# Performance work log

Hardware: AMD Instinct MI355X
Metric: run time of the kernel (lower is better)

The kernel has to match this reference:

```python
import jax, jax.numpy as jnp
import numpy as np

TOPOLOGY = [-1, 0, 0, 0, 1, 2, 3, 4, 5, 6, 7, 8, 9, 9, 9, 12, 13, 14, 16, 17, 18, 19, 20, 21]
JOINT_WEIGHTS = np.ones(24, dtype=np.float32)
B1 = 1.0
B2 = 1.0


def quaternion_to_matrix(q):
    # pytorch3d convention: real part first (w, x, y, z)
    w, x, y, z = q[..., 0], q[..., 1], q[..., 2], q[..., 3]
    two_s = 2.0 / jnp.sum(q * q, axis=-1)
    o = jnp.stack([
        1 - two_s * (y * y + z * z), two_s * (x * y - z * w), two_s * (x * z + y * w),
        two_s * (x * y + z * w), 1 - two_s * (x * x + z * z), two_s * (y * z - x * w),
        two_s * (x * z - y * w), two_s * (y * z + x * w), 1 - two_s * (x * x + y * y),
    ], axis=-1)
    return o.reshape(q.shape[:-1] + (3, 3))


def fk(topology, X_m, X_t):
    # X_m: (bs, T, J*4+3), X_t: (bs, J, 3)
    J = len(topology)
    quat = X_m[..., :-3].reshape(X_m.shape[:-1] + (J, 4))
    local_rot = quaternion_to_matrix(quat)          # (bs, T, J, 3, 3)
    grots = [None] * J
    gtrs = [None] * J
    grots[0] = local_rot[..., 0, :, :]
    gtrs[0] = X_m[..., -3:]                          # root translation
    for i in range(1, J):
        pi = topology[i]
        grots[i] = jnp.matmul(grots[pi], local_rot[..., i, :, :])
        gtrs[i] = jnp.einsum('btij,bj->bti', grots[pi], X_t[:, i]) + gtrs[pi]
    return jnp.stack(grots, axis=-3), jnp.stack(gtrs, axis=-2)


def split_raw_motion(raw_motion):
    position = raw_motion[..., -3:]
    rotation = raw_motion[..., :-3]
    rotation = rotation.reshape(rotation.shape[:-1] + (-1, 4))
    norm = jnp.linalg.norm(rotation, axis=-1, keepdims=True)
    rotation = rotation / jnp.maximum(norm, 1e-12)
    return rotation, position


def weighted_mse(w, a, b):
    # w: (J,), a/b: (bs, T, J, C) -> per-joint weighted mean squared error
    return jnp.mean(w[None, None, :, None] * (a - b) ** 2)


def setup_inputs() -> dict:
    key = jax.random.key(0)
    k1, k2, k3, k4 = jax.random.split(key, 4)
    bs, T, J = 64, 2048, 24
    return {
        'Y_m': jax.random.normal(k1, (bs, T, J * 4 + 3), dtype=jnp.float32),
        'X_m': jax.random.normal(k2, (bs, T, J * 4 + 3), dtype=jnp.float32),
        'Y_t': jax.random.normal(k3, (bs, J, 3), dtype=jnp.float32),
        'X_t': jax.random.normal(k4, (bs, J, 3), dtype=jnp.float32),
    }


def reference(Y_m, X_m, Y_t, X_t):
    w = jnp.asarray(JOINT_WEIGHTS)
    rot_x, pos_x = split_raw_motion(X_m)
    rot_y, pos_y = split_raw_motion(Y_m)
    grot_y, gtr_y = fk(TOPOLOGY, Y_m, Y_t)
    grot_x, gtr_x = fk(TOPOLOGY, X_m, X_t)
    loss_rot = B1 * weighted_mse(w, rot_y, rot_x)
    loss_fk = B2 * (2.5 * weighted_mse(w, gtr_y, gtr_x)
                    + jnp.mean((pos_y - pos_x) ** 2))
    return loss_rot + loss_fk
```

## Files before the change

kernel.cpp:

```cpp
#include <hip/hip_runtime.h>

#define BS 64
#define TT 2048
#define NJ 24
#define ROWF 99
#define BLOCK 128
#define NROWS (BS * TT)

__device__ __forceinline__ void ld4u(const float* __restrict__ p, float* q) {
  const float4 v = *reinterpret_cast<const float4*>(p);
  q[0] = v.x; q[1] = v.y; q[2] = v.z; q[3] = v.w;
}

__device__ __forceinline__ void quat2mat_s(const float* q, float s, float* R) {
  const float w = q[0], x = q[1], y = q[2], z = q[3];
  const float xx = s*x*x, yy = s*y*y, zz = s*z*z;
  const float xy = s*x*y, xz = s*x*z, yz = s*y*z;
  const float xw = s*x*w, yw = s*y*w, zw = s*z*w;
  R[0] = 1.0f - (yy+zz); R[1] = xy - zw;        R[2] = xz + yw;
  R[3] = xy + zw;        R[4] = 1.0f - (xx+zz); R[5] = yz - xw;
  R[6] = xz - yw;        R[7] = yz + xw;        R[8] = 1.0f - (xx+yy);
}

__device__ __forceinline__ void mm3(const float* A, const float* B, float* C) {
#pragma unroll
  for (int r = 0; r < 3; ++r) {
#pragma unroll
    for (int c = 0; c < 3; ++c) {
      C[3*r+c] = fmaf(A[3*r], B[c], fmaf(A[3*r+1], B[3+c], A[3*r+2]*B[6+c]));
    }
  }
}

__global__ __launch_bounds__(BLOCK, 2) void motion_loss_kernel(
    const float* __restrict__ Ym, const float* __restrict__ Xm,
    const float* __restrict__ Yt, const float* __restrict__ Xt,
    float* __restrict__ out) {
  const int tid = threadIdx.x;
  const size_t row = (size_t)blockIdx.x * BLOCK + tid;
  const int b = (int)(row / TT);
  const float* __restrict__ xr = Xm + row * ROWF;
  const float* __restrict__ yr = Ym + row * ROWF;
  const float* __restrict__ tX = Xt + (size_t)b * NJ * 3;
  const float* __restrict__ tY = Yt + (size_t)b * NJ * 3;

  float GX[3][9], GY[3][9], D[3][3];
  float rot_acc = 0.0f, gtr_acc = 0.0f, pos_acc = 0.0f;

  {
    float xq[4], yq[4];
    ld4u(xr, xq); ld4u(yr, yq);
    const float qqx = xq[0]*xq[0] + xq[1]*xq[1] + xq[2]*xq[2] + xq[3]*xq[3];
    const float qqy = yq[0]*yq[0] + yq[1]*yq[1] + yq[2]*yq[2] + yq[3]*yq[3];
    const float ix = 1.0f / fmaxf(sqrtf(qqx), 1e-12f);
    const float iy = 1.0f / fmaxf(sqrtf(qqy), 1e-12f);
    const float r0 = yq[0]*iy - xq[0]*ix, r1 = yq[1]*iy - xq[1]*ix;
    const float r2 = yq[2]*iy - xq[2]*ix, r3 = yq[3]*iy - xq[3]*ix;
    rot_acc += r0*r0 + r1*r1 + r2*r2 + r3*r3;
    quat2mat_s(xq, 2.0f / qqx, GX[0]);
    quat2mat_s(yq, 2.0f / qqy, GY[0]);
    float xp[4], yp[4];
    ld4u(xr + 95, xp); ld4u(yr + 95, yp);
    D[0][0] = yp[1] - xp[1]; D[0][1] = yp[2] - xp[2]; D[0][2] = yp[3] - xp[3];
    const float d2 = D[0][0]*D[0][0] + D[0][1]*D[0][1] + D[0][2]*D[0][2];
    gtr_acc += d2;
    pos_acc = d2;
  }

#define JSTEP(j, PS, NS) do {                                                  \
    float xq[4], yq[4];                                                        \
    ld4u(xr + 4*(j), xq); ld4u(yr + 4*(j), yq);                                \
    const float qqx = xq[0]*xq[0] + xq[1]*xq[1] + xq[2]*xq[2] + xq[3]*xq[3];   \
    const float qqy = yq[0]*yq[0] + yq[1]*yq[1] + yq[2]*yq[2] + yq[3]*yq[3];   \
    const float ix = 1.0f / fmaxf(sqrtf(qqx), 1e-12f);                         \
    const float iy = 1.0f / fmaxf(sqrtf(qqy), 1e-12f);                         \
    const float r0 = yq[0]*iy - xq[0]*ix, r1 = yq[1]*iy - xq[1]*ix;            \
    const float r2 = yq[2]*iy - xq[2]*ix, r3 = yq[3]*iy - xq[3]*ix;            \
    rot_acc += r0*r0 + r1*r1 + r2*r2 + r3*r3;                                  \
    const float tx0 = tX[3*(j)], tx1 = tX[3*(j)+1], tx2 = tX[3*(j)+2];         \
    const float ty0 = tY[3*(j)], ty1 = tY[3*(j)+1], ty2 = tY[3*(j)+2];         \
    const float vx0 = fmaf(GX[PS][0],tx0, fmaf(GX[PS][1],tx1, GX[PS][2]*tx2)); \
    const float vx1 = fmaf(GX[PS][3],tx0, fmaf(GX[PS][4],tx1, GX[PS][5]*tx2)); \
    const float vx2 = fmaf(GX[PS][6],tx0, fmaf(GX[PS][7],tx1, GX[PS][8]*tx2)); \
    const float vy0 = fmaf(GY[PS][0],ty0, fmaf(GY[PS][1],ty1, GY[PS][2]*ty2)); \
    const float vy1 = fmaf(GY[PS][3],ty0, fmaf(GY[PS][4],ty1, GY[PS][5]*ty2)); \
    const float vy2 = fmaf(GY[PS][6],ty0, fmaf(GY[PS][7],ty1, GY[PS][8]*ty2)); \
    const float d0 = D[PS][0] + (vy0 - vx0);                                   \
    const float d1 = D[PS][1] + (vy1 - vx1);                                   \
    const float d2 = D[PS][2] + (vy2 - vx2);                                   \
    gtr_acc += d0*d0 + d1*d1 + d2*d2;                                          \
    float RX[9], RY[9], GnX[9], GnY[9];                                        \
    quat2mat_s(xq, 2.0f / qqx, RX);                                            \
    quat2mat_s(yq, 2.0f / qqy, RY);                                            \
    mm3(GX[PS], RX, GnX);                                                      \
    mm3(GY[PS], RY, GnY);                                                      \
    _Pragma("unroll")                                                          \
    for (int k = 0; k < 9; ++k) { GX[NS][k] = GnX[k]; GY[NS][k] = GnY[k]; }    \
    D[NS][0] = d0; D[NS][1] = d1; D[NS][2] = d2;                               \
  } while (0)

  JSTEP( 1, 0, 1);
  JSTEP( 2, 0, 2);
  JSTEP( 3, 0, 0);
  JSTEP( 4, 1, 1);
  JSTEP( 5, 2, 2);
  JSTEP( 6, 0, 0);
  JSTEP( 7, 1, 1);
  JSTEP( 8, 2, 2);
  JSTEP( 9, 0, 0);
  JSTEP(10, 1, 1);
  JSTEP(11, 2, 2);
  JSTEP(12, 0, 1);
  JSTEP(13, 0, 2);
  JSTEP(14, 0, 0);
  JSTEP(15, 1, 1);
  JSTEP(16, 2, 2);
  JSTEP(17, 0, 0);
  JSTEP(18, 2, 2);
  JSTEP(19, 0, 0);
  JSTEP(20, 2, 2);
  JSTEP(21, 0, 0);
  JSTEP(22, 2, 2);
  JSTEP(23, 0, 0);
#undef JSTEP

  const float c_rot = 1.0f / ((float)NROWS * NJ * 4);
  const float c_gtr = 2.5f / ((float)NROWS * NJ * 3);
  const float c_pos = 1.0f / ((float)NROWS * 3);
  float contrib = c_rot * rot_acc + c_gtr * gtr_acc + c_pos * pos_acc;
#pragma unroll
  for (int o = 32; o > 0; o >>= 1) contrib += __shfl_down(contrib, o, 64);
  if ((tid & 63) == 0) atomicAdd(out, contrib);
}

extern "C" void kernel_launch(void* const* d_in, const int* in_sizes, int n_in,
                              void* d_out, int out_size, void* d_ws, size_t ws_size,
                              hipStream_t stream) {
  const float* Ym = (const float*)d_in[0];
  const float* Xm = (const float*)d_in[1];
  const float* Yt = (const float*)d_in[2];
  const float* Xt = (const float*)d_in[3];
  float* out = (float*)d_out;
  hipMemsetAsync(out, 0, sizeof(float), stream);
  motion_loss_kernel<<<NROWS / BLOCK, BLOCK, 0, stream>>>(Ym, Xm, Yt, Xt, out);
}
```

Baseline: 169.5 us.

## Split X and Y forward kinematics across paired lanes with shuffle differences

Each row is now handled by two adjacent lanes, one walking the X skeleton and one the Y skeleton. The lanes exchange normalized quaternions and joint positions with xor-shuffles to form the differences, and the loss weights are halved because each pair counts its result twice. Per-thread register state drops by about half and twice as many threads run, which should raise occupancy and memory-level parallelism. Bone offsets are staged in shared memory. The cost is extra shuffles per joint, duplicated difference arithmetic, and a strided per-lane access pattern over two input arrays.

```diff
diff --git a/kernel.cpp b/kernel.cpp
--- a/kernel.cpp
+++ b/kernel.cpp
@@ -4,7 +4,8 @@
 #define TT 2048
 #define NJ 24
 #define ROWF 99
-#define BLOCK 128
+#define BLOCK 256
+#define RPB (BLOCK / 2)
 #define NROWS (BS * TT)
 
 __device__ __forceinline__ void ld4u(const float* __restrict__ p, float* q) {
@@ -32,71 +33,72 @@
   }
 }
 
-__global__ __launch_bounds__(BLOCK, 2) void motion_loss_kernel(
+__global__ __launch_bounds__(BLOCK, 4) void motion_loss_kernel(
     const float* __restrict__ Ym, const float* __restrict__ Xm,
     const float* __restrict__ Yt, const float* __restrict__ Xt,
     float* __restrict__ out) {
+  __shared__ float ts[2][NJ * 3];
+
   const int tid = threadIdx.x;
-  const size_t row = (size_t)blockIdx.x * BLOCK + tid;
-  const int b = (int)(row / TT);
-  const float* __restrict__ xr = Xm + row * ROWF;
-  const float* __restrict__ yr = Ym + row * ROWF;
-  const float* __restrict__ tX = Xt + (size_t)b * NJ * 3;
-  const float* __restrict__ tY = Yt + (size_t)b * NJ * 3;
+  const int side = tid & 1;
+  const size_t row = (size_t)blockIdx.x * RPB + (tid >> 1);
+  const int b = (int)(((size_t)blockIdx.x * RPB) / TT);
 
-  float GX[3][9], GY[3][9], D[3][3];
+  if (tid < NJ * 3)                        ts[0][tid]       = Xt[(size_t)b * NJ * 3 + tid];
+  else if (tid >= 128 && tid < 128 + NJ*3) ts[1][tid - 128] = Yt[(size_t)b * NJ * 3 + (tid - 128)];
+  __syncthreads();
+
+  const float* __restrict__ mr = (side ? Ym : Xm) + row * ROWF;
+  const float* __restrict__ tv = ts[side];
+
+  float G[3][9], gtr[3][3];
   float rot_acc = 0.0f, gtr_acc = 0.0f, pos_acc = 0.0f;
 
   {
-    float xq[4], yq[4];
-    ld4u(xr, xq); ld4u(yr, yq);
-    const float qqx = xq[0]*xq[0] + xq[1]*xq[1] + xq[2]*xq[2] + xq[3]*xq[3];
-    const float qqy = yq[0]*yq[0] + yq[1]*yq[1] + yq[2]*yq[2] + yq[3]*yq[3];
-    const float ix = 1.0f / fmaxf(sqrtf(qqx), 1e-12f);
-    const float iy = 1.0f / fmaxf(sqrtf(qqy), 1e-12f);
-    const float r0 = yq[0]*iy - xq[0]*ix, r1 = yq[1]*iy - xq[1]*ix;
-    const float r2 = yq[2]*iy - xq[2]*ix, r3 = yq[3]*iy - xq[3]*ix;
+    float q[4]; ld4u(mr, q);
+    const float qq = q[0]*q[0] + q[1]*q[1] + q[2]*q[2] + q[3]*q[3];
+    const float in = 1.0f / fmaxf(sqrtf(qq), 1e-12f);
+    const float n0 = q[0]*in, n1 = q[1]*in, n2 = q[2]*in, n3 = q[3]*in;
+    const float r0 = n0 - __shfl_xor(n0, 1, 64);
+    const float r1 = n1 - __shfl_xor(n1, 1, 64);
+    const float r2 = n2 - __shfl_xor(n2, 1, 64);
+    const float r3 = n3 - __shfl_xor(n3, 1, 64);
     rot_acc += r0*r0 + r1*r1 + r2*r2 + r3*r3;
-    quat2mat_s(xq, 2.0f / qqx, GX[0]);
-    quat2mat_s(yq, 2.0f / qqy, GY[0]);
-    float xp[4], yp[4];
-    ld4u(xr + 95, xp); ld4u(yr + 95, yp);
-    D[0][0] = yp[1] - xp[1]; D[0][1] = yp[2] - xp[2]; D[0][2] = yp[3] - xp[3];
-    const float d2 = D[0][0]*D[0][0] + D[0][1]*D[0][1] + D[0][2]*D[0][2];
-    gtr_acc += d2;
-    pos_acc = d2;
+    quat2mat_s(q, 2.0f / qq, G[0]);
+    float p[4]; ld4u(mr + 95, p);
+    gtr[0][0] = p[1]; gtr[0][1] = p[2]; gtr[0][2] = p[3];
+    const float d0 = gtr[0][0] - __shfl_xor(gtr[0][0], 1, 64);
+    const float d1 = gtr[0][1] - __shfl_xor(gtr[0][1], 1, 64);
+    const float d2 = gtr[0][2] - __shfl_xor(gtr[0][2], 1, 64);
+    const float dd = d0*d0 + d1*d1 + d2*d2;
+    gtr_acc += dd;
+    pos_acc  = dd;
   }
 
 #define JSTEP(j, PS, NS) do {                                                  \
-    float xq[4], yq[4];                                                        \
-    ld4u(xr + 4*(j), xq); ld4u(yr + 4*(j), yq);                                \
-    const float qqx = xq[0]*xq[0] + xq[1]*xq[1] + xq[2]*xq[2] + xq[3]*xq[3];   \
-    const float qqy = yq[0]*yq[0] + yq[1]*yq[1] + yq[2]*yq[2] + yq[3]*yq[3];   \
-    const float ix = 1.0f / fmaxf(sqrtf(qqx), 1e-12f);                         \
-    const float iy = 1.0f / fmaxf(sqrtf(qqy), 1e-12f);                         \
-    const float r0 = yq[0]*iy - xq[0]*ix, r1 = yq[1]*iy - xq[1]*ix;            \
-    const float r2 = yq[2]*iy - xq[2]*ix, r3 = yq[3]*iy - xq[3]*ix;            \
+    float q[4]; ld4u(mr + 4*(j), q);                                           \
+    const float qq = q[0]*q[0] + q[1]*q[1] + q[2]*q[2] + q[3]*q[3];            \
+    const float in = 1.0f / fmaxf(sqrtf(qq), 1e-12f);                          \
+    const float n0 = q[0]*in, n1 = q[1]*in, n2 = q[2]*in, n3 = q[3]*in;        \
+    const float r0 = n0 - __shfl_xor(n0, 1, 64);                               \
+    const float r1 = n1 - __shfl_xor(n1, 1, 64);                               \
+    const float r2 = n2 - __shfl_xor(n2, 1, 64);                               \
+    const float r3 = n3 - __shfl_xor(n3, 1, 64);                               \
     rot_acc += r0*r0 + r1*r1 + r2*r2 + r3*r3;                                  \
-    const float tx0 = tX[3*(j)], tx1 = tX[3*(j)+1], tx2 = tX[3*(j)+2];         \
-    const float ty0 = tY[3*(j)], ty1 = tY[3*(j)+1], ty2 = tY[3*(j)+2];         \
-    const float vx0 = fmaf(GX[PS][0],tx0, fmaf(GX[PS][1],tx1, GX[PS][2]*tx2)); \
-    const float vx1 = fmaf(GX[PS][3],tx0, fmaf(GX[PS][4],tx1, GX[PS][5]*tx2)); \
-    const float vx2 = fmaf(GX[PS][6],tx0, fmaf(GX[PS][7],tx1, GX[PS][8]*tx2)); \
-    const float vy0 = fmaf(GY[PS][0],ty0, fmaf(GY[PS][1],ty1, GY[PS][2]*ty2)); \
-    const float vy1 = fmaf(GY[PS][3],ty0, fmaf(GY[PS][4],ty1, GY[PS][5]*ty2)); \
-    const float vy2 = fmaf(GY[PS][6],ty0, fmaf(GY[PS][7],ty1, GY[PS][8]*ty2)); \
-    const float d0 = D[PS][0] + (vy0 - vx0);                                   \
-    const float d1 = D[PS][1] + (vy1 - vx1);                                   \
-    const float d2 = D[PS][2] + (vy2 - vx2);                                   \
+    const float t0 = tv[3*(j)], t1 = tv[3*(j)+1], t2 = tv[3*(j)+2];            \
+    const float v0 = fmaf(G[PS][0],t0, fmaf(G[PS][1],t1, fmaf(G[PS][2],t2, gtr[PS][0]))); \
+    const float v1 = fmaf(G[PS][3],t0, fmaf(G[PS][4],t1, fmaf(G[PS][5],t2, gtr[PS][1]))); \
+    const float v2 = fmaf(G[PS][6],t0, fmaf(G[PS][7],t1, fmaf(G[PS][8],t2, gtr[PS][2]))); \
+    const float d0 = v0 - __shfl_xor(v0, 1, 64);                               \
+    const float d1 = v1 - __shfl_xor(v1, 1, 64);                               \
+    const float d2 = v2 - __shfl_xor(v2, 1, 64);                               \
     gtr_acc += d0*d0 + d1*d1 + d2*d2;                                          \
-    float RX[9], RY[9], GnX[9], GnY[9];                                        \
-    quat2mat_s(xq, 2.0f / qqx, RX);                                            \
-    quat2mat_s(yq, 2.0f / qqy, RY);                                            \
-    mm3(GX[PS], RX, GnX);                                                      \
-    mm3(GY[PS], RY, GnY);                                                      \
+    float R[9], Gn[9];                                                         \
+    quat2mat_s(q, 2.0f / qq, R);                                               \
+    mm3(G[PS], R, Gn);                                                         \
     _Pragma("unroll")                                                          \
-    for (int k = 0; k < 9; ++k) { GX[NS][k] = GnX[k]; GY[NS][k] = GnY[k]; }    \
-    D[NS][0] = d0; D[NS][1] = d1; D[NS][2] = d2;                               \
+    for (int k = 0; k < 9; ++k) G[NS][k] = Gn[k];                              \
+    gtr[NS][0] = v0; gtr[NS][1] = v1; gtr[NS][2] = v2;                         \
   } while (0)
 
   JSTEP( 1, 0, 1);
@@ -124,9 +126,9 @@
   JSTEP(23, 0, 0);
 #undef JSTEP
 
-  const float c_rot = 1.0f / ((float)NROWS * NJ * 4);
-  const float c_gtr = 2.5f / ((float)NROWS * NJ * 3);
-  const float c_pos = 1.0f / ((float)NROWS * 3);
+  const float c_rot = 0.5f / ((float)NROWS * NJ * 4);
+  const float c_gtr = 1.25f / ((float)NROWS * NJ * 3);
+  const float c_pos = 0.5f / ((float)NROWS * 3);
   float contrib = c_rot * rot_acc + c_gtr * gtr_acc + c_pos * pos_acc;
 #pragma unroll
   for (int o = 32; o > 0; o >>= 1) contrib += __shfl_down(contrib, o, 64);
@@ -142,5 +144,5 @@
   const float* Xt = (const float*)d_in[3];
   float* out = (float*)d_out;
   hipMemsetAsync(out, 0, sizeof(float), stream);
-  motion_loss_kernel<<<NROWS / BLOCK, BLOCK, 0, stream>>>(Ym, Xm, Yt, Xt, out);
+  motion_loss_kernel<<<NROWS / RPB, BLOCK, 0, stream>>>(Ym, Xm, Yt, Xt, out);
 }
```

Result: slower. 198.4 us (+17.0%).

## Split each row's kinematic tree across two wavefronts and stage offsets in LDS

Applied to the files above, without the earlier changes.

Each motion row is now handled by two threads in different wavefronts. One walks the spine and the left and right arm chains, the other walks the two leg chains after recomputing the shared spine prefix (joints 3, 6, 9) without accumulating. This shortens the serial dependency chain per thread, cuts live rotation state from three to two matrices, and allows four blocks per SM in the launch bounds. The per-batch joint offsets are staged in shared memory. The cost is the redundant spine recomputation and duplicate loads of the root quaternion and position.

```diff
diff --git a/kernel.cpp b/kernel.cpp
--- a/kernel.cpp
+++ b/kernel.cpp
@@ -4,7 +4,8 @@
 #define TT 2048
 #define NJ 24
 #define ROWF 99
-#define BLOCK 128
+#define BLOCK 256
+#define RPB 128
 #define NROWS (BS * TT)
 
 __device__ __forceinline__ void ld4u(const float* __restrict__ p, float* q) {
@@ -32,51 +33,50 @@
   }
 }
 
-__global__ __launch_bounds__(BLOCK, 2) void motion_loss_kernel(
-    const float* __restrict__ Ym, const float* __restrict__ Xm,
-    const float* __restrict__ Yt, const float* __restrict__ Xt,
-    float* __restrict__ out) {
-  const int tid = threadIdx.x;
-  const size_t row = (size_t)blockIdx.x * BLOCK + tid;
-  const int b = (int)(row / TT);
-  const float* __restrict__ xr = Xm + row * ROWF;
-  const float* __restrict__ yr = Ym + row * ROWF;
-  const float* __restrict__ tX = Xt + (size_t)b * NJ * 3;
-  const float* __restrict__ tY = Yt + (size_t)b * NJ * 3;
-
-  float GX[3][9], GY[3][9], D[3][3];
-  float rot_acc = 0.0f, gtr_acc = 0.0f, pos_acc = 0.0f;
+template<int PART>
+__device__ __forceinline__ void fk_part(const float* __restrict__ xr,
+                                        const float* __restrict__ yr,
+                                        const float* __restrict__ tX,
+                                        const float* __restrict__ tY,
+                                        float& rot_acc, float& gtr_acc, float& pos_acc) {
+  float GX[2][9], GY[2][9], D[2][3];
 
   {
     float xq[4], yq[4];
     ld4u(xr, xq); ld4u(yr, yq);
     const float qqx = xq[0]*xq[0] + xq[1]*xq[1] + xq[2]*xq[2] + xq[3]*xq[3];
     const float qqy = yq[0]*yq[0] + yq[1]*yq[1] + yq[2]*yq[2] + yq[3]*yq[3];
-    const float ix = 1.0f / fmaxf(sqrtf(qqx), 1e-12f);
-    const float iy = 1.0f / fmaxf(sqrtf(qqy), 1e-12f);
-    const float r0 = yq[0]*iy - xq[0]*ix, r1 = yq[1]*iy - xq[1]*ix;
-    const float r2 = yq[2]*iy - xq[2]*ix, r3 = yq[3]*iy - xq[3]*ix;
-    rot_acc += r0*r0 + r1*r1 + r2*r2 + r3*r3;
+    if (PART == 0) {
+      const float ix = 1.0f / fmaxf(sqrtf(qqx), 1e-12f);
+      const float iy = 1.0f / fmaxf(sqrtf(qqy), 1e-12f);
+      const float r0 = yq[0]*iy - xq[0]*ix, r1 = yq[1]*iy - xq[1]*ix;
+      const float r2 = yq[2]*iy - xq[2]*ix, r3 = yq[3]*iy - xq[3]*ix;
+      rot_acc += r0*r0 + r1*r1 + r2*r2 + r3*r3;
+    }
     quat2mat_s(xq, 2.0f / qqx, GX[0]);
     quat2mat_s(yq, 2.0f / qqy, GY[0]);
     float xp[4], yp[4];
     ld4u(xr + 95, xp); ld4u(yr + 95, yp);
     D[0][0] = yp[1] - xp[1]; D[0][1] = yp[2] - xp[2]; D[0][2] = yp[3] - xp[3];
-    const float d2 = D[0][0]*D[0][0] + D[0][1]*D[0][1] + D[0][2]*D[0][2];
-    gtr_acc += d2;
-    pos_acc = d2;
+    if (PART == 0) {
+      const float dd = D[0][0]*D[0][0] + D[0][1]*D[0][1] + D[0][2]*D[0][2];
+      gtr_acc += dd;
+      pos_acc  = dd;
+    }
   }
 
-#define JSTEP(j, PS, NS) do {                                                  \
+#define JSTEP(j, PS, NS, ACC) do {                                             \
     float xq[4], yq[4];                                                        \
     ld4u(xr + 4*(j), xq); ld4u(yr + 4*(j), yq);                                \
     const float qqx = xq[0]*xq[0] + xq[1]*xq[1] + xq[2]*xq[2] + xq[3]*xq[3];   \
     const float qqy = yq[0]*yq[0] + yq[1]*yq[1] + yq[2]*yq[2] + yq[3]*yq[3];   \
-    const float ix = 1.0f / fmaxf(sqrtf(qqx), 1e-12f);                         \
-    const float iy = 1.0f / fmaxf(sqrtf(qqy), 1e-12f);                         \
-    const float r0 = yq[0]*iy - xq[0]*ix, r1 = yq[1]*iy - xq[1]*ix;            \
-    const float r2 = yq[2]*iy - xq[2]*ix, r3 = yq[3]*iy - xq[3]*ix;            \
-    rot_acc += r0*r0 + r1*r1 + r2*r2 + r3*r3;                                  \
+    if (ACC) {                                                                 \
+      const float ix = 1.0f / fmaxf(sqrtf(qqx), 1e-12f);                       \
+      const float iy = 1.0f / fmaxf(sqrtf(qqy), 1e-12f);                       \
+      const float r0 = yq[0]*iy - xq[0]*ix, r1 = yq[1]*iy - xq[1]*ix;          \
+      const float r2 = yq[2]*iy - xq[2]*ix, r3 = yq[3]*iy - xq[3]*ix;          \
+      rot_acc += r0*r0 + r1*r1 + r2*r2 + r3*r3;                                \
+    }                                                                          \
     const float tx0 = tX[3*(j)], tx1 = tX[3*(j)+1], tx2 = tX[3*(j)+2];         \
     const float ty0 = tY[3*(j)], ty1 = tY[3*(j)+1], ty2 = tY[3*(j)+2];         \
     const float vx0 = fmaf(GX[PS][0],tx0, fmaf(GX[PS][1],tx1, GX[PS][2]*tx2)); \
@@ -88,7 +88,7 @@
     const float d0 = D[PS][0] + (vy0 - vx0);                                   \
     const float d1 = D[PS][1] + (vy1 - vx1);                                   \
     const float d2 = D[PS][2] + (vy2 - vx2);                                   \
-    gtr_acc += d0*d0 + d1*d1 + d2*d2;                                          \
+    if (ACC) gtr_acc += d0*d0 + d1*d1 + d2*d2;                                 \
     float RX[9], RY[9], GnX[9], GnY[9];                                        \
     quat2mat_s(xq, 2.0f / qqx, RX);                                            \
     quat2mat_s(yq, 2.0f / qqy, RY);                                            \
@@ -99,30 +99,41 @@
     D[NS][0] = d0; D[NS][1] = d1; D[NS][2] = d2;                               \
   } while (0)
 
-  JSTEP( 1, 0, 1);
-  JSTEP( 2, 0, 2);
-  JSTEP( 3, 0, 0);
-  JSTEP( 4, 1, 1);
-  JSTEP( 5, 2, 2);
-  JSTEP( 6, 0, 0);
-  JSTEP( 7, 1, 1);
-  JSTEP( 8, 2, 2);
-  JSTEP( 9, 0, 0);
-  JSTEP(10, 1, 1);
-  JSTEP(11, 2, 2);
-  JSTEP(12, 0, 1);
-  JSTEP(13, 0, 2);
-  JSTEP(14, 0, 0);
-  JSTEP(15, 1, 1);
-  JSTEP(16, 2, 2);
-  JSTEP(17, 0, 0);
-  JSTEP(18, 2, 2);
-  JSTEP(19, 0, 0);
-  JSTEP(20, 2, 2);
-  JSTEP(21, 0, 0);
-  JSTEP(22, 2, 2);
-  JSTEP(23, 0, 0);
+  if (PART == 0) {
+    JSTEP( 1, 0, 1, 1); JSTEP( 4, 1, 1, 1); JSTEP( 7, 1, 1, 1); JSTEP(10, 1, 1, 1);
+    JSTEP( 2, 0, 1, 1); JSTEP( 5, 1, 1, 1); JSTEP( 8, 1, 1, 1); JSTEP(11, 1, 1, 1);
+    JSTEP( 3, 0, 0, 1); JSTEP( 6, 0, 0, 1); JSTEP( 9, 0, 0, 1);
+    JSTEP(12, 0, 0, 1); JSTEP(15, 0, 0, 1);
+  } else {
+    JSTEP( 3, 0, 0, 0); JSTEP( 6, 0, 0, 0); JSTEP( 9, 0, 0, 0);
+    JSTEP(13, 0, 1, 1); JSTEP(16, 1, 1, 1); JSTEP(18, 1, 1, 1); JSTEP(20, 1, 1, 1); JSTEP(22, 1, 1, 1);
+    JSTEP(14, 0, 1, 1); JSTEP(17, 1, 1, 1); JSTEP(19, 1, 1, 1); JSTEP(21, 1, 1, 1); JSTEP(23, 1, 1, 1);
+  }
 #undef JSTEP
+}
+
+__global__ __launch_bounds__(BLOCK, 4) void motion_loss_kernel(
+    const float* __restrict__ Ym, const float* __restrict__ Xm,
+    const float* __restrict__ Yt, const float* __restrict__ Xt,
+    float* __restrict__ out) {
+  __shared__ float ts[2][NJ * 3];
+
+  const int tid = threadIdx.x;
+  const int wv = tid >> 6;
+  const int part = wv & 1;
+  const size_t row = (size_t)blockIdx.x * RPB + (size_t)(wv >> 1) * 64 + (tid & 63);
+  const int b = (int)(((size_t)blockIdx.x * RPB) / TT);
+
+  if (tid < NJ * 3)                        ts[0][tid]       = Xt[(size_t)b * NJ * 3 + tid];
+  else if (tid >= 128 && tid < 128 + NJ*3) ts[1][tid - 128] = Yt[(size_t)b * NJ * 3 + (tid - 128)];
+  __syncthreads();
+
+  const float* __restrict__ xr = Xm + row * ROWF;
+  const float* __restrict__ yr = Ym + row * ROWF;
+
+  float rot_acc = 0.0f, gtr_acc = 0.0f, pos_acc = 0.0f;
+  if (part == 0) fk_part<0>(xr, yr, ts[0], ts[1], rot_acc, gtr_acc, pos_acc);
+  else           fk_part<1>(xr, yr, ts[0], ts[1], rot_acc, gtr_acc, pos_acc);
 
   const float c_rot = 1.0f / ((float)NROWS * NJ * 4);
   const float c_gtr = 2.5f / ((float)NROWS * NJ * 3);
@@ -142,5 +153,5 @@
   const float* Xt = (const float*)d_in[3];
   float* out = (float*)d_out;
   hipMemsetAsync(out, 0, sizeof(float), stream);
-  motion_loss_kernel<<<NROWS / BLOCK, BLOCK, 0, stream>>>(Ym, Xm, Yt, Xt, out);
+  motion_loss_kernel<<<NROWS / RPB, BLOCK, 0, stream>>>(Ym, Xm, Yt, Xt, out);
 }
```

After: 425.0 us. 151% more time.
